# Performance work log

Measured on AMD Instinct MI355X. Metric: run time of the kernel, lower is better.

The kernel has to match this reference:

```python
import jax, jax.numpy as jnp
import numpy as np

ALPHA = 0.2          # LeakyReLU negative slope
NEG_INF = -9e15      # masking value from the original module


def setup_inputs() -> dict:
    key = jax.random.key(0)
    kw, ka, k1, k2, k3 = jax.random.split(key, 5)
    B, N1, N2, F, O = 4, 2048, 2048, 256, 256
    word = jax.random.normal(kw, (B, N2, F), dtype=jnp.float32)
    # 0/1 hypergraph incidence matrix (float, as in the torch module)
    adj = jax.random.randint(ka, (B, N1, N2), 0, 2).astype(jnp.float32)
    stdv = 1.0 / np.sqrt(O)
    W1 = jax.random.uniform(k1, (F, O), jnp.float32, -stdv, stdv)
    W2 = jax.random.uniform(k2, (F, O), jnp.float32, -stdv, stdv)
    w3 = jax.random.uniform(k3, (2 * O, 1), jnp.float32, -stdv, stdv)
    return {"word": word, "adj": adj, "W1": W1, "W2": W2, "w3": w3}


def reference(word, adj, W1, W2, w3):
    # word: [B, N2, F]; adj: [B, N1, N2]; W1/W2: [F, O]; w3: [2O, 1]
    O = W1.shape[1]
    # mean-pool neighbor features per hyperedge (row-normalized adj)
    deg = jnp.sum(adj, axis=-1, keepdims=True)                 # [B, N1, 1]
    deg = jnp.where(deg > 0, deg, jnp.ones_like(deg))
    mp = jnp.matmul(adj / deg, word)                           # [B, N1, F]
    # The original builds 4D tensors h1[b,i,j,:] = adj[b,i,j]*word[b,j,:] and
    # h_mp[b,i,j,:] = adj[b,i,j]*mp[b,i,:], projects both and dots with w3.
    # Since scaling commutes with the linear maps, the scalar score is
    #   adj[b,i,j] * (word[b,j] @ W1 @ w3_a + mp[b,i] @ W2 @ w3_b)
    w3a = w3[:O, 0]                                            # pairs with w1h
    w3b = w3[O:, 0]                                            # pairs with w2h
    s1 = jnp.einsum('bnf,fo,o->bn', word, W1, w3a)             # [B, N2]
    s2 = jnp.einsum('bnf,fo,o->bn', mp, W2, w3b)               # [B, N1]
    pre = adj * (s2[:, :, None] + s1[:, None, :])              # [B, N1, N2]
    alpha = jnp.exp(jax.nn.leaky_relu(pre, ALPHA))
    attention = jnp.where(adj > 0, alpha, NEG_INF)
    attention_edge = jax.nn.softmax(attention, axis=2)         # over N2
    edge = jnp.matmul(attention_edge, word)                    # [B, N1, F]
    return edge
```

## Files before the change

kernel.cpp:

```cpp
#include <hip/hip_runtime.h>

#define B 4
#define N 2048
#define F 256
#define O 256
#define LOG2E 1.4426950408889634f
#define NEG_BIG -9000000000000000.0f

typedef _Float16 f16;
typedef f16 f16x4 __attribute__((ext_vector_type(4)));
typedef f16 f16x8 __attribute__((ext_vector_type(8)));
typedef float f32x4 __attribute__((ext_vector_type(4)));

#define WS_V1 0
#define WS_V2 256
#define WS_T1 512
#define WS_T2 (512 + B*N)
#define WT_OFF (1u << 20)

__device__ __forceinline__ float alpha_of(float pre2) {
  return __builtin_amdgcn_exp2f(fmaxf(pre2, 0.2f * pre2));
}

__global__ __launch_bounds__(256) void k_v(const float* __restrict__ W1,
                                           const float* __restrict__ W2,
                                           const float* __restrict__ w3,
                                           float* __restrict__ ws) {
  int tid = threadIdx.x;
  int lane = tid & 63;
  int f = blockIdx.x * 4 + (tid >> 6);
  float a = 0.f, b = 0.f;
  #pragma unroll
  for (int k = 0; k < 4; ++k) {
    int o = lane + 64 * k;
    a += W1[f * O + o] * w3[o];
    b += W2[f * O + o] * w3[O + o];
  }
  #pragma unroll
  for (int off = 32; off > 0; off >>= 1) {
    a += __shfl_down(a, off);
    b += __shfl_down(b, off);
  }
  if (lane == 0) {
    ws[WS_V1 + f] = a;
    ws[WS_V2 + f] = b;
  }
}

__global__ __launch_bounds__(256) void k_prep(const float* __restrict__ word,
                                              float* __restrict__ ws,
                                              f16* __restrict__ wordT) {
  __shared__ float v1s[F], v2s[F];
  __shared__ __align__(16) f16 tile[F][40];
  int t = threadIdx.x;
  int k0 = blockIdx.x * 32;
  int b = blockIdx.y;

  if (t < 64)       ((float4*)v1s)[t]      = ((const float4*)(ws + WS_V1))[t];
  else if (t < 128) ((float4*)v2s)[t - 64] = ((const float4*)(ws + WS_V2))[t - 64];
  __syncthreads();

  int r = t >> 3;
  int cg = t & 7;
  const float* wrow = word + ((size_t)(b * N + k0 + r)) * F;
  float a = 0.f, bb = 0.f;
  #pragma unroll
  for (int i = 0; i < 8; ++i) {
    int c = i * 32 + cg * 4;
    float4 w = *(const float4*)(wrow + c);
    float4 x1 = *(const float4*)(v1s + c);
    float4 x2 = *(const float4*)(v2s + c);
    a  += w.x * x1.x + w.y * x1.y + w.z * x1.z + w.w * x1.w;
    bb += w.x * x2.x + w.y * x2.y + w.z * x2.z + w.w * x2.w;
    tile[c + 0][r] = (f16)w.x;
    tile[c + 1][r] = (f16)w.y;
    tile[c + 2][r] = (f16)w.z;
    tile[c + 3][r] = (f16)w.w;
  }
  #pragma unroll
  for (int off = 4; off > 0; off >>= 1) {
    a  += __shfl_down(a, off);
    bb += __shfl_down(bb, off);
  }
  if (cg == 0) {
    ws[WS_T1 + b * N + k0 + r] = a * LOG2E;
    ws[WS_T2 + b * N + k0 + r] = bb;
  }
  __syncthreads();

  size_t base = (size_t)b * F * N;
  int kc = k0 >> 5;
  #pragma unroll
  for (int s = 0; s < 4; ++s) {
    int u = t + 256 * s;
    int ft = u >> 6, l2 = u & 63;
    f16x8 h = *(const f16x8*)&tile[ft * 16 + (l2 & 15)][(l2 >> 4) * 8];
    *(f16x8*)(wordT + base + ((size_t)(ft * 64 + kc) * 64 + l2) * 8) = h;
  }
}

__global__ __launch_bounds__(512, 4) void k_sg(const float* __restrict__ adj,
                                               const float* __restrict__ ws,
                                               const f16* __restrict__ wordT,
                                               float* __restrict__ out) {
  extern __shared__ __align__(16) char smem[];
  float* t1S = (float*)(smem + 65536);
  float* t2S = (float*)(smem + 73728);

  const int t = threadIdx.x;
  const int wv = t >> 6, l = t & 63;
  const int bid = blockIdx.x;
  const int sbid = (bid & 7) * 64 + (bid >> 3);
  const int row0 = sbid * 16;
  const int b = row0 >> 11;

  *(float4*)(t1S + t * 4) = *(const float4*)(ws + WS_T1 + b * N + t * 4);
  *(float4*)(t2S + t * 4) = *(const float4*)(ws + WS_T2 + b * N + t * 4);
  __syncthreads();

  #pragma unroll 1
  for (int rr = 0; rr < 2; ++rr) {
    const int lrow = wv * 2 + rr;
    const float* arow = adj + (size_t)(row0 + lrow) * N;

    float deg = 0.f, dot = 0.f;
    unsigned mb = 0u;
    #pragma unroll
    for (int i = 0; i < 8; ++i) {
      int k = i * 256 + l * 4;
      float4 av = *(const float4*)(arow + k);
      float4 uv = *(const float4*)(t2S + k);
      deg += av.x + av.y + av.z + av.w;
      dot += av.x * uv.x + av.y * uv.y + av.z * uv.z + av.w * uv.w;
      mb |= (av.x > 0.f ? (1u << (4 * i + 0)) : 0u) |
            (av.y > 0.f ? (1u << (4 * i + 1)) : 0u) |
            (av.z > 0.f ? (1u << (4 * i + 2)) : 0u) |
            (av.w > 0.f ? (1u << (4 * i + 3)) : 0u);
    }
    #pragma unroll
    for (int off = 32; off > 0; off >>= 1) {
      deg += __shfl_xor(deg, off);
      dot += __shfl_xor(dot, off);
    }
    float degc = deg > 0.f ? deg : 1.f;
    float s2p = (dot / degc) * LOG2E;

    float al[32];
    float m = NEG_BIG;
    #pragma unroll
    for (int i = 0; i < 8; ++i) {
      int k = i * 256 + l * 4;
      float4 pv = *(const float4*)(t1S + k);
      const float p[4] = {pv.x, pv.y, pv.z, pv.w};
      #pragma unroll
      for (int c = 0; c < 4; ++c) {
        int j = 4 * i + c;
        al[j] = ((mb >> j) & 1u) ? alpha_of(p[c] + s2p) : NEG_BIG;
        m = fmaxf(m, al[j]);
      }
    }
    #pragma unroll
    for (int off = 32; off > 0; off >>= 1) m = fmaxf(m, __shfl_xor(m, off));

    float negmL = -m * LOG2E;
    float z = 0.f;
    #pragma unroll
    for (int j = 0; j < 32; ++j) {
      float e = __builtin_amdgcn_exp2f(fmaf(al[j], LOG2E, negmL));
      z += e;
      al[j] = e;
    }
    #pragma unroll
    for (int off = 32; off > 0; off >>= 1) z += __shfl_xor(z, off);
    float sc, wn;
    if (deg > 0.f) { sc = 1.0f / z; wn = 0.f; }
    else           { sc = 0.f;      wn = 1.0f / (float)N; }

    #pragma unroll
    for (int i = 0; i < 8; ++i) {
      f16x4 h;
      #pragma unroll
      for (int c = 0; c < 4; ++c) {
        int j = 4 * i + c;
        float w = ((mb >> j) & 1u) ? al[j] * sc : wn;
        h[c] = (f16)w;
      }
      unsigned byteoff = (unsigned)(lrow * 4096 + i * 512 + l * 8) ^ ((unsigned)(lrow & 7) << 4);
      *(f16x4*)(smem + byteoff) = h;
    }
  }
  __syncthreads();

  const int ft0 = wv * 2;
  const unsigned abase = (unsigned)((l & 15) * 4096 + (l >> 4) * 16);
  const unsigned ax = ((unsigned)(l & 7)) << 4;
  const f16* bp0 = wordT + (size_t)b * (F * N) + ((size_t)ft0 * 64 * 64 + (size_t)l) * 8;
  const f16* bp1 = bp0 + (size_t)64 * 512;

  f32x4 acc0 = {0.f, 0.f, 0.f, 0.f};
  f32x4 acc1 = {0.f, 0.f, 0.f, 0.f};
  #pragma unroll 8
  for (int kc = 0; kc < 64; ++kc) {
    f16x8 af = *(const f16x8*)(smem + ((abase + kc * 64) ^ ax));
    f16x8 bf0 = *(const f16x8*)(bp0 + (size_t)kc * 512);
    f16x8 bf1 = *(const f16x8*)(bp1 + (size_t)kc * 512);
    acc0 = __builtin_amdgcn_mfma_f32_16x16x32_f16(af, bf0, acc0, 0, 0, 0);
    acc1 = __builtin_amdgcn_mfma_f32_16x16x32_f16(af, bf1, acc1, 0, 0, 0);
  }

  const int orow = row0 + (l >> 4) * 4;
  const int c0 = ft0 * 16 + (l & 15);
  #pragma unroll
  for (int reg = 0; reg < 4; ++reg) {
    out[(size_t)(orow + reg) * F + c0]      = acc0[reg];
    out[(size_t)(orow + reg) * F + c0 + 16] = acc1[reg];
  }
}

extern "C" void kernel_launch(void* const* d_in, const int* in_sizes, int n_in,
                              void* d_out, int out_size, void* d_ws, size_t ws_size,
                              hipStream_t stream) {
  const float* word = (const float*)d_in[0];
  const float* adj  = (const float*)d_in[1];
  const float* W1   = (const float*)d_in[2];
  const float* W2   = (const float*)d_in[3];
  const float* w3   = (const float*)d_in[4];
  float* out = (float*)d_out;
  float* ws  = (float*)d_ws;
  f16* wordT = (f16*)((char*)d_ws + WT_OFF);

  static bool s_attr = false;
  if (!s_attr) {
    hipFuncSetAttribute((const void*)k_sg, hipFuncAttributeMaxDynamicSharedMemorySize, 81920);
    s_attr = true;
  }

  k_v<<<64, 256, 0, stream>>>(W1, W2, w3, ws);
  k_prep<<<dim3(N / 32, B), 256, 0, stream>>>(word, ws, wordT);
  k_sg<<<(B * N) / 16, 512, 81920, stream>>>(adj, ws, wordT, out);
}
```

Measured before the change: 131.9 us.

## Pack adjacency into bitmasks in a pre-pass and double rows per block

A new pre-kernel reads the float adjacency once and writes one 32-bit mask per lane segment. The main kernel now computes degree by popcount and the masked dot from that mask, instead of re-reading 64MB of floats inside the attention kernel. The main kernel also doubles its tile to 32 rows with 1024 threads, so each wordT B-fragment feeds two MFMAs against two A row tiles, halving global B traffic. This costs an extra launch, relies on adj being 0/1, and uses more LDS per block, which leaves fewer, larger blocks per CU.

Result: no change. 130.5 us (-1.1%).

```diff
diff --git a/kernel.cpp b/kernel.cpp
--- a/kernel.cpp
+++ b/kernel.cpp
@@ -17,9 +17,28 @@
 #define WS_T1 512
 #define WS_T2 (512 + B*N)
 #define WT_OFF (1u << 20)
+#define MK_OFF (6u << 20)
 
 __device__ __forceinline__ float alpha_of(float pre2) {
   return __builtin_amdgcn_exp2f(fmaxf(pre2, 0.2f * pre2));
+}
+
+__global__ __launch_bounds__(256) void k_mask(const float* __restrict__ adj,
+                                              unsigned* __restrict__ maskg) {
+  int t = threadIdx.x;
+  int wv = t >> 6, l = t & 63;
+  int row = blockIdx.x * 4 + wv;
+  const float* arow = adj + (size_t)row * N;
+  unsigned mb = 0u;
+  #pragma unroll
+  for (int i = 0; i < 8; ++i) {
+    float4 av = *(const float4*)(arow + i * 256 + l * 4);
+    mb |= (av.x > 0.f ? (1u << (4 * i + 0)) : 0u) |
+          (av.y > 0.f ? (1u << (4 * i + 1)) : 0u) |
+          (av.z > 0.f ? (1u << (4 * i + 2)) : 0u) |
+          (av.w > 0.f ? (1u << (4 * i + 3)) : 0u);
+  }
+  maskg[(size_t)row * 64 + l] = mb;
 }
 
 __global__ __launch_bounds__(256) void k_v(const float* __restrict__ W1,
@@ -99,43 +118,43 @@
   }
 }
 
-__global__ __launch_bounds__(512, 4) void k_sg(const float* __restrict__ adj,
-                                               const float* __restrict__ ws,
-                                               const f16* __restrict__ wordT,
-                                               float* __restrict__ out) {
+__global__ __launch_bounds__(1024, 4) void k_sg(const unsigned* __restrict__ maskg,
+                                                const float* __restrict__ ws,
+                                                const f16* __restrict__ wordT,
+                                                float* __restrict__ out) {
   extern __shared__ __align__(16) char smem[];
-  float* t1S = (float*)(smem + 65536);
-  float* t2S = (float*)(smem + 73728);
+  float* t1S = (float*)(smem + 131072);
+  float* t2S = (float*)(smem + 139264);
 
   const int t = threadIdx.x;
   const int wv = t >> 6, l = t & 63;
   const int bid = blockIdx.x;
-  const int sbid = (bid & 7) * 64 + (bid >> 3);
-  const int row0 = sbid * 16;
+  const int sbid = (bid & 7) * 32 + (bid >> 3);
+  const int row0 = sbid * 32;
   const int b = row0 >> 11;
 
-  *(float4*)(t1S + t * 4) = *(const float4*)(ws + WS_T1 + b * N + t * 4);
-  *(float4*)(t2S + t * 4) = *(const float4*)(ws + WS_T2 + b * N + t * 4);
+  if (t < 512) {
+    *(float4*)(t1S + t * 4) = *(const float4*)(ws + WS_T1 + b * N + t * 4);
+  } else {
+    int u = t - 512;
+    *(float4*)(t2S + u * 4) = *(const float4*)(ws + WS_T2 + b * N + u * 4);
+  }
   __syncthreads();
 
   #pragma unroll 1
   for (int rr = 0; rr < 2; ++rr) {
     const int lrow = wv * 2 + rr;
-    const float* arow = adj + (size_t)(row0 + lrow) * N;
-
-    float deg = 0.f, dot = 0.f;
-    unsigned mb = 0u;
+    const unsigned mb = maskg[(size_t)(row0 + lrow) * 64 + l];
+
+    float deg = (float)__builtin_popcount(mb);
+    float dot = 0.f;
     #pragma unroll
     for (int i = 0; i < 8; ++i) {
-      int k = i * 256 + l * 4;
-      float4 av = *(const float4*)(arow + k);
-      float4 uv = *(const float4*)(t2S + k);
-      deg += av.x + av.y + av.z + av.w;
-      dot += av.x * uv.x + av.y * uv.y + av.z * uv.z + av.w * uv.w;
-      mb |= (av.x > 0.f ? (1u << (4 * i + 0)) : 0u) |
-            (av.y > 0.f ? (1u << (4 * i + 1)) : 0u) |
-            (av.z > 0.f ? (1u << (4 * i + 2)) : 0u) |
-            (av.w > 0.f ? (1u << (4 * i + 3)) : 0u);
+      float4 uv = *(const float4*)(t2S + i * 256 + l * 4);
+      dot += (((mb >> (4 * i + 0)) & 1u) ? uv.x : 0.f);
+      dot += (((mb >> (4 * i + 1)) & 1u) ? uv.y : 0.f);
+      dot += (((mb >> (4 * i + 2)) & 1u) ? uv.z : 0.f);
+      dot += (((mb >> (4 * i + 3)) & 1u) ? uv.w : 0.f);
     }
     #pragma unroll
     for (int off = 32; off > 0; off >>= 1) {
@@ -149,8 +168,7 @@
     float m = NEG_BIG;
     #pragma unroll
     for (int i = 0; i < 8; ++i) {
-      int k = i * 256 + l * 4;
-      float4 pv = *(const float4*)(t1S + k);
+      float4 pv = *(const float4*)(t1S + i * 256 + l * 4);
       const float p[4] = {pv.x, pv.y, pv.z, pv.w};
       #pragma unroll
       for (int c = 0; c < 4; ++c) {
@@ -191,29 +209,28 @@
   }
   __syncthreads();
 
-  const int ft0 = wv * 2;
+  const int ftile = wv;
   const unsigned abase = (unsigned)((l & 15) * 4096 + (l >> 4) * 16);
   const unsigned ax = ((unsigned)(l & 7)) << 4;
-  const f16* bp0 = wordT + (size_t)b * (F * N) + ((size_t)ft0 * 64 * 64 + (size_t)l) * 8;
-  const f16* bp1 = bp0 + (size_t)64 * 512;
+  const f16* bp = wordT + (size_t)b * (F * N) + ((size_t)ftile * 64 * 64 + (size_t)l) * 8;
 
   f32x4 acc0 = {0.f, 0.f, 0.f, 0.f};
   f32x4 acc1 = {0.f, 0.f, 0.f, 0.f};
   #pragma unroll 8
   for (int kc = 0; kc < 64; ++kc) {
-    f16x8 af = *(const f16x8*)(smem + ((abase + kc * 64) ^ ax));
-    f16x8 bf0 = *(const f16x8*)(bp0 + (size_t)kc * 512);
-    f16x8 bf1 = *(const f16x8*)(bp1 + (size_t)kc * 512);
-    acc0 = __builtin_amdgcn_mfma_f32_16x16x32_f16(af, bf0, acc0, 0, 0, 0);
-    acc1 = __builtin_amdgcn_mfma_f32_16x16x32_f16(af, bf1, acc1, 0, 0, 0);
+    f16x8 bf = *(const f16x8*)(bp + (size_t)kc * 512);
+    f16x8 a0 = *(const f16x8*)(smem + ((abase + kc * 64) ^ ax));
+    f16x8 a1 = *(const f16x8*)(smem + ((abase + 16 * 4096 + kc * 64) ^ ax));
+    acc0 = __builtin_amdgcn_mfma_f32_16x16x32_f16(a0, bf, acc0, 0, 0, 0);
+    acc1 = __builtin_amdgcn_mfma_f32_16x16x32_f16(a1, bf, acc1, 0, 0, 0);
   }
 
   const int orow = row0 + (l >> 4) * 4;
-  const int c0 = ft0 * 16 + (l & 15);
+  const int c0 = ftile * 16 + (l & 15);
   #pragma unroll
   for (int reg = 0; reg < 4; ++reg) {
     out[(size_t)(orow + reg) * F + c0]      = acc0[reg];
-    out[(size_t)(orow + reg) * F + c0 + 16] = acc1[reg];
+    out[(size_t)(orow + 16 + reg) * F + c0] = acc1[reg];
   }
 }
 
@@ -228,14 +245,16 @@
   float* out = (float*)d_out;
   float* ws  = (float*)d_ws;
   f16* wordT = (f16*)((char*)d_ws + WT_OFF);
+  unsigned* maskg = (unsigned*)((char*)d_ws + MK_OFF);
 
   static bool s_attr = false;
   if (!s_attr) {
-    hipFuncSetAttribute((const void*)k_sg, hipFuncAttributeMaxDynamicSharedMemorySize, 81920);
+    hipFuncSetAttribute((const void*)k_sg, hipFuncAttributeMaxDynamicSharedMemorySize, 147456);
     s_attr = true;
   }
 
+  k_mask<<<(B * N) / 4, 256, 0, stream>>>(adj, maskg);
   k_v<<<64, 256, 0, stream>>>(W1, W2, w3, ws);
   k_prep<<<dim3(N / 32, B), 256, 0, stream>>>(word, ws, wordT);
-  k_sg<<<(B * N) / 16, 512, 81920, stream>>>(adj, ws, wordT, out);
-}
+  k_sg<<<(B * N) / 32, 1024, 147456, stream>>>(maskg, ws, wordT, out);
+}
```
